# Optimization experiments

Measured on AMD Instinct MI355X. Metric: run time of the kernel, lower is better.

## Reference

```python
import jax, jax.numpy as jnp
import numpy as np

B = 512          # batch of visual features
VF_D = 4096      # visual feature dim (VGG fc7)
HID_D = 2048     # hidden dim
EMB_D = 300      # order-embedding / label-vector dim
N_LABELS = 2000  # number of GT label vectors


def setup_inputs() -> dict:
    key = jax.random.key(0)
    ks = jax.random.split(key, 4)
    vfs = jax.random.normal(ks[0], (B, VF_D), dtype=jnp.float32)
    W1 = jax.random.normal(ks[1], (VF_D, HID_D), dtype=jnp.float32) * (1.0 / np.sqrt(VF_D))
    b1 = jnp.zeros((HID_D,), dtype=jnp.float32)
    W2 = jax.random.normal(ks[2], (HID_D, EMB_D), dtype=jnp.float32) * (1.0 / np.sqrt(HID_D))
    b2 = jnp.zeros((EMB_D,), dtype=jnp.float32)
    gt_label_vecs = jax.random.normal(ks[3], (N_LABELS, EMB_D), dtype=jnp.float32)
    return {"vfs": vfs, "W1": W1, "b1": b1, "W2": W2, "b2": b2,
            "gt_label_vecs": gt_label_vecs}


def reference(vfs, W1, b1, W2, b2, gt_label_vecs):
    # hidden_layer: ReLU -> (Dropout, identity at eval) -> Linear
    vf_hidden = jnp.dot(jax.nn.relu(vfs), W1) + b1            # [B, HID_D]
    # embedding_layer: ReLU -> Linear
    vf_emb = jnp.dot(jax.nn.relu(vf_hidden), W2) + b2         # [B, EMB_D]
    # order_sim(hypers=gt_label_vecs, hypos=vf_emb):
    #   score = -|| clamp(hypo - hyper, min=0) ||^2, batched over all pairs
    diff = jax.nn.relu(vf_emb[:, None, :] - gt_label_vecs[None, :, :])  # [B, N, D]
    score_stack = -jnp.sum(diff * diff, axis=-1)              # [B, N_LABELS]
    return score_stack, vf_emb
```

## Files before the change

### kernel.cpp

```cpp
#include <hip/hip_runtime.h>

#define B_SZ   512
#define VFD    4096
#define HIDD   2048
#define EMBD   300
#define NLAB   2000
#define NPAD   320

#define G1_SPLIT 4
#define G2_SPLIT 8
#define SD_SPLIT 4

typedef __attribute__((ext_vector_type(8))) short short8x;
typedef __attribute__((ext_vector_type(4))) float f32x4;
typedef __attribute__((ext_vector_type(8))) unsigned short ushort8;
typedef __attribute__((ext_vector_type(4))) unsigned short ushort4x;

typedef const __attribute__((address_space(1))) unsigned int* gas_t;
typedef __attribute__((address_space(3))) unsigned int* las_t;

__device__ inline unsigned short f2bf(float x) {
    unsigned u = __float_as_uint(x);
    u += 0x7FFF + ((u >> 16) & 1);
    return (unsigned short)(u >> 16);
}

__global__ __launch_bounds__(256) void prep_kernel(
    const float* __restrict__ vfs, unsigned short* __restrict__ Xb,
    const float* __restrict__ W1, unsigned short* __restrict__ W1T,
    const float* __restrict__ W2, unsigned short* __restrict__ W2T)
{
    __shared__ float tile[64][65];
    const int tid = threadIdx.x;
    const int blk = blockIdx.x;

    if (blk < 1024) {
        const int i = (blk * 256 + tid) * 8;
        float4 a = *(const float4*)&vfs[i];
        float4 b = *(const float4*)&vfs[i + 4];
        ushort8 o;
        o[0] = f2bf(fmaxf(a.x, 0.f)); o[1] = f2bf(fmaxf(a.y, 0.f));
        o[2] = f2bf(fmaxf(a.z, 0.f)); o[3] = f2bf(fmaxf(a.w, 0.f));
        o[4] = f2bf(fmaxf(b.x, 0.f)); o[5] = f2bf(fmaxf(b.y, 0.f));
        o[6] = f2bf(fmaxf(b.z, 0.f)); o[7] = f2bf(fmaxf(b.w, 0.f));
        *(ushort8*)&Xb[i] = o;
        return;
    }

    const float* in; unsigned short* out; int N, ldK, bx, by;
    if (blk < 3072) {
        const int b = blk - 1024;
        in = W1; out = W1T; N = HIDD; ldK = VFD; bx = b & 31; by = b >> 5;
    } else {
        const int b = blk - 3072;
        in = W2; out = W2T; N = EMBD; ldK = HIDD; bx = b % 5; by = b / 5;
    }
    const int n0 = bx * 64, k0 = by * 64;

    #pragma unroll
    for (int i = 0; i < 4; ++i) {
        const int s = tid + 256 * i;
        const int kr = s >> 4, nc = (s & 15) * 4;
        float4 v = {0.f, 0.f, 0.f, 0.f};
        if (n0 + nc < N) v = *(const float4*)&in[(size_t)(k0 + kr) * N + n0 + nc];
        tile[kr][nc + 0] = v.x; tile[kr][nc + 1] = v.y;
        tile[kr][nc + 2] = v.z; tile[kr][nc + 3] = v.w;
    }
    __syncthreads();

    const int row = tid >> 2, kq = (tid & 3) * 16;
    ushort8 o0, o1;
    #pragma unroll
    for (int j = 0; j < 8; ++j) o0[j] = f2bf(tile[kq + j][row]);
    #pragma unroll
    for (int j = 0; j < 8; ++j) o1[j] = f2bf(tile[kq + 8 + j][row]);
    const size_t off = (size_t)(n0 + row) * ldK + k0 + kq;
    *(ushort8*)&out[off]     = o0;
    *(ushort8*)&out[off + 8] = o1;
}

__global__ __launch_bounds__(256) void gemm1_kernel(
    const unsigned short* __restrict__ A,
    const unsigned short* __restrict__ Bt,
    float* __restrict__ Cpart)
{
    __shared__ unsigned short As[2][2048];
    __shared__ unsigned short Bs[2][4096];

    const int tid = threadIdx.x;
    const int m0 = blockIdx.y * 64, n0 = blockIdx.x * 128;
    const int kbase = blockIdx.z * (VFD / G1_SPLIT);

    const unsigned short* ga = A + (size_t)(m0 + (tid & 63)) * VFD + kbase + (tid >> 6) * 8;
    const int brow = tid & 127, boct = tid >> 7;
    const unsigned short* gb0 = Bt + (size_t)(n0 + brow) * VFD + kbase + boct * 8;
    const unsigned short* gb1 = gb0 + 16;

    const int lane = tid & 63;
    const int wave = tid >> 6;
    const int wm = (wave & 1) * 32;
    const int wn = (wave >> 1) * 64;
    const int q = lane >> 4, l15 = lane & 15;

    f32x4 acc[2][4];
    #pragma unroll
    for (int r = 0; r < 2; ++r)
        #pragma unroll
        for (int c = 0; c < 4; ++c) acc[r][c] = (f32x4){0.f,0.f,0.f,0.f};

    __builtin_amdgcn_global_load_lds((gas_t)(const void*)ga,
                                     (las_t)(void*)&As[0][tid * 8], 16, 0, 0);
    __builtin_amdgcn_global_load_lds((gas_t)(const void*)gb0,
                                     (las_t)(void*)&Bs[0][tid * 8], 16, 0, 0);
    __builtin_amdgcn_global_load_lds((gas_t)(const void*)gb1,
                                     (las_t)(void*)&Bs[0][(tid + 256) * 8], 16, 0, 0);

    const int iters = (VFD / G1_SPLIT) / 32;
    for (int t = 0; t < iters; ++t) {
        const int cur = t & 1, nxt = cur ^ 1;
        __syncthreads();

        if (t + 1 < iters) {
            const int ko = (t + 1) * 32;
            __builtin_amdgcn_global_load_lds((gas_t)(const void*)(ga + ko),
                                             (las_t)(void*)&As[nxt][tid * 8], 16, 0, 0);
            __builtin_amdgcn_global_load_lds((gas_t)(const void*)(gb0 + ko),
                                             (las_t)(void*)&Bs[nxt][tid * 8], 16, 0, 0);
            __builtin_amdgcn_global_load_lds((gas_t)(const void*)(gb1 + ko),
                                             (las_t)(void*)&Bs[nxt][(tid + 256) * 8], 16, 0, 0);
        }

        short8x a0 = *(short8x*)&As[cur][(q * 64 + wm +      l15) * 8];
        short8x a1 = *(short8x*)&As[cur][(q * 64 + wm + 16 + l15) * 8];
        #pragma unroll
        for (int c = 0; c < 4; ++c) {
            short8x b = *(short8x*)&Bs[cur][(q * 128 + wn + c * 16 + l15) * 8];
            acc[0][c] = __builtin_amdgcn_mfma_f32_16x16x32_bf16(a0, b, acc[0][c], 0, 0, 0);
            acc[1][c] = __builtin_amdgcn_mfma_f32_16x16x32_bf16(a1, b, acc[1][c], 0, 0, 0);
        }
    }

    float* Cz = Cpart + (size_t)blockIdx.z * B_SZ * HIDD;
    #pragma unroll
    for (int r = 0; r < 2; ++r) {
        #pragma unroll
        for (int g = 0; g < 4; ++g) {
            const int rr = m0 + wm + r * 16 + q * 4 + g;
            #pragma unroll
            for (int c = 0; c < 4; ++c)
                Cz[(size_t)rr * HIDD + n0 + wn + c * 16 + l15] = acc[r][c][g];
        }
    }
}

template<int LDA, int LDB, int LDC, int KCHUNK>
__global__ __launch_bounds__(256) void gemm_bf16_kernel(
    const unsigned short* __restrict__ A,
    const unsigned short* __restrict__ Bt,
    float* __restrict__ Cpart, int M)
{
    __shared__ unsigned short As[2][2048];
    __shared__ unsigned short Bs[2][2048];

    const int tid = threadIdx.x;
    const int m0 = blockIdx.y * 64, n0 = blockIdx.x * 64;
    const int kbase = blockIdx.z * KCHUNK;

    const unsigned short* ga = A  + (size_t)(m0 + (tid & 63)) * LDA + kbase + (tid >> 6) * 8;
    const unsigned short* gb = Bt + (size_t)(n0 + (tid & 63)) * LDB + kbase + (tid >> 6) * 8;

    const int lane = tid & 63;
    const int wave = tid >> 6;
    const int wm = (wave & 1) * 32;
    const int wn = (wave >> 1) * 32;
    const int q = lane >> 4, l15 = lane & 15;

    f32x4 acc00 = {0.f,0.f,0.f,0.f}, acc01 = {0.f,0.f,0.f,0.f};
    f32x4 acc10 = {0.f,0.f,0.f,0.f}, acc11 = {0.f,0.f,0.f,0.f};

    __builtin_amdgcn_global_load_lds((gas_t)(const void*)ga,
                                     (las_t)(void*)&As[0][tid * 8], 16, 0, 0);
    __builtin_amdgcn_global_load_lds((gas_t)(const void*)gb,
                                     (las_t)(void*)&Bs[0][tid * 8], 16, 0, 0);

    const int iters = KCHUNK / 32;
    for (int t = 0; t < iters; ++t) {
        const int cur = t & 1, nxt = cur ^ 1;
        __syncthreads();

        if (t + 1 < iters) {
            __builtin_amdgcn_global_load_lds((gas_t)(const void*)(ga + (t + 1) * 32),
                                             (las_t)(void*)&As[nxt][tid * 8], 16, 0, 0);
            __builtin_amdgcn_global_load_lds((gas_t)(const void*)(gb + (t + 1) * 32),
                                             (las_t)(void*)&Bs[nxt][tid * 8], 16, 0, 0);
        }

        short8x a0 = *(short8x*)&As[cur][(q * 64 + wm +      l15) * 8];
        short8x a1 = *(short8x*)&As[cur][(q * 64 + wm + 16 + l15) * 8];
        short8x b0 = *(short8x*)&Bs[cur][(q * 64 + wn +      l15) * 8];
        short8x b1 = *(short8x*)&Bs[cur][(q * 64 + wn + 16 + l15) * 8];
        acc00 = __builtin_amdgcn_mfma_f32_16x16x32_bf16(a0, b0, acc00, 0, 0, 0);
        acc01 = __builtin_amdgcn_mfma_f32_16x16x32_bf16(a0, b1, acc01, 0, 0, 0);
        acc10 = __builtin_amdgcn_mfma_f32_16x16x32_bf16(a1, b0, acc10, 0, 0, 0);
        acc11 = __builtin_amdgcn_mfma_f32_16x16x32_bf16(a1, b1, acc11, 0, 0, 0);
    }

    float* Cz = Cpart + (size_t)blockIdx.z * M * LDC;
    #pragma unroll
    for (int r = 0; r < 4; ++r) {
        const int rr = m0 + wm + q * 4 + r;
        const int cc = n0 + wn + l15;
        Cz[(size_t)rr * LDC + cc]             = acc00[r];
        Cz[(size_t)rr * LDC + cc + 16]        = acc01[r];
        Cz[(size_t)(rr + 16) * LDC + cc]      = acc10[r];
        Cz[(size_t)(rr + 16) * LDC + cc + 16] = acc11[r];
    }
}

__global__ __launch_bounds__(256) void reduce_h_kernel(
    const float* __restrict__ Hpart, const float* __restrict__ b1,
    unsigned short* __restrict__ Hb)
{
    const int i = (blockIdx.x * 256 + threadIdx.x) * 4;
    const int col = i & (HIDD - 1);
    float4 s = *(const float4*)&b1[col];
    #pragma unroll
    for (int z = 0; z < G1_SPLIT; ++z) {
        float4 p = *(const float4*)&Hpart[(size_t)z * B_SZ * HIDD + i];
        s.x += p.x; s.y += p.y; s.z += p.z; s.w += p.w;
    }
    ushort4x o;
    o[0] = f2bf(fmaxf(s.x, 0.f));
    o[1] = f2bf(fmaxf(s.y, 0.f));
    o[2] = f2bf(fmaxf(s.z, 0.f));
    o[3] = f2bf(fmaxf(s.w, 0.f));
    *(ushort4x*)&Hb[i] = o;
}

__global__ __launch_bounds__(256) void reduce_e_zero_kernel(
    const float* __restrict__ Epart, const float* __restrict__ b2,
    float* __restrict__ E, float* __restrict__ scores)
{
    const int blk = blockIdx.x;
    if (blk < 600) {
        const int gid = blk * 256 + threadIdx.x;
        if (gid >= B_SZ * EMBD) return;
        const int m = gid / EMBD, n = gid - m * EMBD;
        float v = b2[n];
        #pragma unroll
        for (int z = 0; z < G2_SPLIT; ++z)
            v += Epart[(size_t)z * B_SZ * NPAD + m * NPAD + n];
        E[gid] = v;
    } else {
        const int i = ((blk - 600) * 256 + threadIdx.x) * 4;
        if (i < B_SZ * NLAB) {
            float4 z = {0.f, 0.f, 0.f, 0.f};
            *(float4*)&scores[i] = z;
        }
    }
}

__global__ __launch_bounds__(128) void scores_part_kernel(
    const float* __restrict__ E, const float* __restrict__ G,
    float* __restrict__ scores)
{
    __shared__ float Gs[64][44];

    const int tid = threadIdx.x;
    const int tx = tid & 15, ty = tid >> 4;
    const int n0 = blockIdx.x * 64, b0 = blockIdx.y * 32;
    const int dbase = blockIdx.z * (NPAD / SD_SPLIT);

    float acc[4][4] = {};

    for (int dc = 0; dc < NPAD / SD_SPLIT; dc += 40) {
        const int d0 = dbase + dc;
        __syncthreads();
        #pragma unroll
        for (int i = 0; i < 5; ++i) {
            const int s = tid + 128 * i;
            const int row = s / 10, qd = (s - row * 10) * 4;
            const int d = d0 + qd;
            const int n = n0 + row;
            float4 v = {0.f, 0.f, 0.f, 0.f};
            if (n < NLAB && d < EMBD) v = *(const float4*)&G[(size_t)n * EMBD + d];
            *(float4*)&Gs[row][qd] = v;
        }
        __syncthreads();

        #pragma unroll 2
        for (int d = 0; d < 40; d += 4) {
            const int dd = d0 + d;
            float4 e[4];
            if (dd < EMBD) {
                #pragma unroll
                for (int r = 0; r < 4; ++r)
                    e[r] = *(const float4*)&E[(size_t)(b0 + ty * 4 + r) * EMBD + dd];
            } else {
                #pragma unroll
                for (int r = 0; r < 4; ++r) e[r] = make_float4(0.f, 0.f, 0.f, 0.f);
            }
            #pragma unroll
            for (int c = 0; c < 4; ++c) {
                float4 g = *(float4*)&Gs[tx + 16 * c][d];
                #pragma unroll
                for (int r = 0; r < 4; ++r) {
                    float t;
                    t = fmaxf(e[r].x - g.x, 0.f); acc[r][c] += t * t;
                    t = fmaxf(e[r].y - g.y, 0.f); acc[r][c] += t * t;
                    t = fmaxf(e[r].z - g.z, 0.f); acc[r][c] += t * t;
                    t = fmaxf(e[r].w - g.w, 0.f); acc[r][c] += t * t;
                }
            }
        }
    }

    #pragma unroll
    for (int r = 0; r < 4; ++r) {
        const int b = b0 + ty * 4 + r;
        #pragma unroll
        for (int c = 0; c < 4; ++c) {
            const int n = n0 + tx + 16 * c;
            if (n < NLAB) atomicAdd(&scores[(size_t)b * NLAB + n], -acc[r][c]);
        }
    }
}

extern "C" void kernel_launch(void* const* d_in, const int* in_sizes, int n_in,
                              void* d_out, int out_size, void* d_ws, size_t ws_size,
                              hipStream_t stream)
{
    const float* vfs = (const float*)d_in[0];
    const float* W1  = (const float*)d_in[1];
    const float* b1  = (const float*)d_in[2];
    const float* W2  = (const float*)d_in[3];
    const float* b2  = (const float*)d_in[4];
    const float* G   = (const float*)d_in[5];

    float* out    = (float*)d_out;
    float* scores = out;
    float* E      = out + (size_t)B_SZ * NLAB;

    char* ws = (char*)d_ws;
    unsigned short* Xb  = (unsigned short*)(ws);
    unsigned short* W1T = (unsigned short*)(ws + 4194304);
    unsigned short* W2T = (unsigned short*)(ws + 20971520);
    unsigned short* Hb  = (unsigned short*)(ws + 22282240);
    float*          Hpart = (float*)(ws + 24379392);
    float*          Epart = (float*)(ws + 41156608);

    prep_kernel<<<3232, 256, 0, stream>>>(vfs, Xb, W1, W1T, W2, W2T);

    gemm1_kernel<<<dim3(16, 8, G1_SPLIT), 256, 0, stream>>>(Xb, W1T, Hpart);
    reduce_h_kernel<<<1024, 256, 0, stream>>>(Hpart, b1, Hb);

    gemm_bf16_kernel<HIDD, HIDD, NPAD, HIDD / G2_SPLIT>
        <<<dim3(5, 8, G2_SPLIT), 256, 0, stream>>>(Hb, W2T, Epart, B_SZ);
    reduce_e_zero_kernel<<<1624, 256, 0, stream>>>(Epart, b2, E, scores);

    scores_part_kernel<<<dim3(32, 16, SD_SPLIT), 128, 0, stream>>>(E, G, scores);
}
```

Measured before the change: 174.5 us.

## Deepen GEMM K-tiles to 64, pack bf16 in transpose, move score zeroing to prep

Both bf16 MFMA GEMMs now stage 64-wide K tiles per double-buffered iteration instead of 32. This halves the number of barriers and loop iterations at the cost of twice the LDS per block. The weight-transpose prep converts to bf16 before the LDS transpose, packing pairs of K values into 32-bit words, which cuts LDS footprint and shared-memory traffic. Zeroing of the score buffer moves from the E-reduction kernel into extra blocks of the prep kernel, so it runs off the critical path.

```diff
diff --git a/kernel.cpp b/kernel.cpp
--- a/kernel.cpp
+++ b/kernel.cpp
@@ -28,9 +28,10 @@
 __global__ __launch_bounds__(256) void prep_kernel(
     const float* __restrict__ vfs, unsigned short* __restrict__ Xb,
     const float* __restrict__ W1, unsigned short* __restrict__ W1T,
-    const float* __restrict__ W2, unsigned short* __restrict__ W2T)
-{
-    __shared__ float tile[64][65];
+    const float* __restrict__ W2, unsigned short* __restrict__ W2T,
+    float* __restrict__ scores)
+{
+    __shared__ unsigned int Lds[64][34];
     const int tid = threadIdx.x;
     const int blk = blockIdx.x;
 
@@ -46,6 +47,14 @@
         *(ushort8*)&Xb[i] = o;
         return;
     }
+    if (blk >= 3232) {
+        const int i = ((blk - 3232) * 256 + tid) * 4;
+        if (i < B_SZ * NLAB) {
+            float4 z = {0.f, 0.f, 0.f, 0.f};
+            *(float4*)&scores[i] = z;
+        }
+        return;
+    }
 
     const float* in; unsigned short* out; int N, ldK, bx, by;
     if (blk < 3072) {
@@ -58,25 +67,31 @@
     const int n0 = bx * 64, k0 = by * 64;
 
     #pragma unroll
-    for (int i = 0; i < 4; ++i) {
+    for (int i = 0; i < 2; ++i) {
         const int s = tid + 256 * i;
-        const int kr = s >> 4, nc = (s & 15) * 4;
-        float4 v = {0.f, 0.f, 0.f, 0.f};
-        if (n0 + nc < N) v = *(const float4*)&in[(size_t)(k0 + kr) * N + n0 + nc];
-        tile[kr][nc + 0] = v.x; tile[kr][nc + 1] = v.y;
-        tile[kr][nc + 2] = v.z; tile[kr][nc + 3] = v.w;
+        const int kp = s >> 4, nq = s & 15;
+        const int n = n0 + nq * 4;
+        float4 v0 = {0.f,0.f,0.f,0.f}, v1 = {0.f,0.f,0.f,0.f};
+        if (n < N) {
+            v0 = *(const float4*)&in[(size_t)(k0 + 2 * kp)     * N + n];
+            v1 = *(const float4*)&in[(size_t)(k0 + 2 * kp + 1) * N + n];
+        }
+        Lds[nq*4+0][kp] = (unsigned)f2bf(v0.x) | ((unsigned)f2bf(v1.x) << 16);
+        Lds[nq*4+1][kp] = (unsigned)f2bf(v0.y) | ((unsigned)f2bf(v1.y) << 16);
+        Lds[nq*4+2][kp] = (unsigned)f2bf(v0.z) | ((unsigned)f2bf(v1.z) << 16);
+        Lds[nq*4+3][kp] = (unsigned)f2bf(v0.w) | ((unsigned)f2bf(v1.w) << 16);
     }
     __syncthreads();
 
-    const int row = tid >> 2, kq = (tid & 3) * 16;
-    ushort8 o0, o1;
-    #pragma unroll
-    for (int j = 0; j < 8; ++j) o0[j] = f2bf(tile[kq + j][row]);
-    #pragma unroll
-    for (int j = 0; j < 8; ++j) o1[j] = f2bf(tile[kq + 8 + j][row]);
-    const size_t off = (size_t)(n0 + row) * ldK + k0 + kq;
-    *(ushort8*)&out[off]     = o0;
-    *(ushort8*)&out[off + 8] = o1;
+    #pragma unroll
+    for (int i = 0; i < 2; ++i) {
+        const int c = tid + 256 * i;
+        const int n = c >> 3, oct = c & 7;
+        uint2 lo = *(uint2*)&Lds[n][oct * 4];
+        uint2 hi = *(uint2*)&Lds[n][oct * 4 + 2];
+        uint4 v = make_uint4(lo.x, lo.y, hi.x, hi.y);
+        *(uint4*)&out[(size_t)(n0 + n) * ldK + k0 + oct * 8] = v;
+    }
 }
 
 __global__ __launch_bounds__(256) void gemm1_kernel(
@@ -84,17 +99,15 @@
     const unsigned short* __restrict__ Bt,
     float* __restrict__ Cpart)
 {
-    __shared__ unsigned short As[2][2048];
-    __shared__ unsigned short Bs[2][4096];
+    __shared__ unsigned short As[2][4096];
+    __shared__ unsigned short Bs[2][8192];
 
     const int tid = threadIdx.x;
     const int m0 = blockIdx.y * 64, n0 = blockIdx.x * 128;
     const int kbase = blockIdx.z * (VFD / G1_SPLIT);
 
     const unsigned short* ga = A + (size_t)(m0 + (tid & 63)) * VFD + kbase + (tid >> 6) * 8;
-    const int brow = tid & 127, boct = tid >> 7;
-    const unsigned short* gb0 = Bt + (size_t)(n0 + brow) * VFD + kbase + boct * 8;
-    const unsigned short* gb1 = gb0 + 16;
+    const unsigned short* gb = Bt + (size_t)(n0 + (tid & 127)) * VFD + kbase + (tid >> 7) * 8;
 
     const int lane = tid & 63;
     const int wave = tid >> 6;
@@ -108,35 +121,43 @@
         #pragma unroll
         for (int c = 0; c < 4; ++c) acc[r][c] = (f32x4){0.f,0.f,0.f,0.f};
 
-    __builtin_amdgcn_global_load_lds((gas_t)(const void*)ga,
-                                     (las_t)(void*)&As[0][tid * 8], 16, 0, 0);
-    __builtin_amdgcn_global_load_lds((gas_t)(const void*)gb0,
-                                     (las_t)(void*)&Bs[0][tid * 8], 16, 0, 0);
-    __builtin_amdgcn_global_load_lds((gas_t)(const void*)gb1,
-                                     (las_t)(void*)&Bs[0][(tid + 256) * 8], 16, 0, 0);
-
-    const int iters = (VFD / G1_SPLIT) / 32;
+    #pragma unroll
+    for (int i = 0; i < 2; ++i)
+        __builtin_amdgcn_global_load_lds((gas_t)(const void*)(ga + i * 32),
+                                         (las_t)(void*)&As[0][(tid + 256 * i) * 8], 16, 0, 0);
+    #pragma unroll
+    for (int i = 0; i < 4; ++i)
+        __builtin_amdgcn_global_load_lds((gas_t)(const void*)(gb + i * 16),
+                                         (las_t)(void*)&Bs[0][(tid + 256 * i) * 8], 16, 0, 0);
+
+    const int iters = (VFD / G1_SPLIT) / 64;
     for (int t = 0; t < iters; ++t) {
         const int cur = t & 1, nxt = cur ^ 1;
         __syncthreads();
 
         if (t + 1 < iters) {
-            const int ko = (t + 1) * 32;
-            __builtin_amdgcn_global_load_lds((gas_t)(const void*)(ga + ko),
-                                             (las_t)(void*)&As[nxt][tid * 8], 16, 0, 0);
-            __builtin_amdgcn_global_load_lds((gas_t)(const void*)(gb0 + ko),
-                                             (las_t)(void*)&Bs[nxt][tid * 8], 16, 0, 0);
-            __builtin_amdgcn_global_load_lds((gas_t)(const void*)(gb1 + ko),
-                                             (las_t)(void*)&Bs[nxt][(tid + 256) * 8], 16, 0, 0);
-        }
-
-        short8x a0 = *(short8x*)&As[cur][(q * 64 + wm +      l15) * 8];
-        short8x a1 = *(short8x*)&As[cur][(q * 64 + wm + 16 + l15) * 8];
-        #pragma unroll
-        for (int c = 0; c < 4; ++c) {
-            short8x b = *(short8x*)&Bs[cur][(q * 128 + wn + c * 16 + l15) * 8];
-            acc[0][c] = __builtin_amdgcn_mfma_f32_16x16x32_bf16(a0, b, acc[0][c], 0, 0, 0);
-            acc[1][c] = __builtin_amdgcn_mfma_f32_16x16x32_bf16(a1, b, acc[1][c], 0, 0, 0);
+            const int ko = (t + 1) * 64;
+            #pragma unroll
+            for (int i = 0; i < 2; ++i)
+                __builtin_amdgcn_global_load_lds((gas_t)(const void*)(ga + ko + i * 32),
+                                                 (las_t)(void*)&As[nxt][(tid + 256 * i) * 8], 16, 0, 0);
+            #pragma unroll
+            for (int i = 0; i < 4; ++i)
+                __builtin_amdgcn_global_load_lds((gas_t)(const void*)(gb + ko + i * 16),
+                                                 (las_t)(void*)&Bs[nxt][(tid + 256 * i) * 8], 16, 0, 0);
+        }
+
+        #pragma unroll
+        for (int kk = 0; kk < 2; ++kk) {
+            const int oct = kk * 4 + q;
+            short8x a0 = *(short8x*)&As[cur][(oct * 64 + wm +      l15) * 8];
+            short8x a1 = *(short8x*)&As[cur][(oct * 64 + wm + 16 + l15) * 8];
+            #pragma unroll
+            for (int c = 0; c < 4; ++c) {
+                short8x b = *(short8x*)&Bs[cur][(oct * 128 + wn + c * 16 + l15) * 8];
+                acc[0][c] = __builtin_amdgcn_mfma_f32_16x16x32_bf16(a0, b, acc[0][c], 0, 0, 0);
+                acc[1][c] = __builtin_amdgcn_mfma_f32_16x16x32_bf16(a1, b, acc[1][c], 0, 0, 0);
+            }
         }
     }
 
@@ -159,8 +180,8 @@
     const unsigned short* __restrict__ Bt,
     float* __restrict__ Cpart, int M)
 {
-    __shared__ unsigned short As[2][2048];
-    __shared__ unsigned short Bs[2][2048];
+    __shared__ unsigned short As[2][4096];
+    __shared__ unsigned short Bs[2][4096];
 
     const int tid = threadIdx.x;
     const int m0 = blockIdx.y * 64, n0 = blockIdx.x * 64;
@@ -178,31 +199,42 @@
     f32x4 acc00 = {0.f,0.f,0.f,0.f}, acc01 = {0.f,0.f,0.f,0.f};
     f32x4 acc10 = {0.f,0.f,0.f,0.f}, acc11 = {0.f,0.f,0.f,0.f};
 
-    __builtin_amdgcn_global_load_lds((gas_t)(const void*)ga,
-                                     (las_t)(void*)&As[0][tid * 8], 16, 0, 0);
-    __builtin_amdgcn_global_load_lds((gas_t)(const void*)gb,
-                                     (las_t)(void*)&Bs[0][tid * 8], 16, 0, 0);
-
-    const int iters = KCHUNK / 32;
+    #pragma unroll
+    for (int i = 0; i < 2; ++i) {
+        __builtin_amdgcn_global_load_lds((gas_t)(const void*)(ga + i * 32),
+                                         (las_t)(void*)&As[0][(tid + 256 * i) * 8], 16, 0, 0);
+        __builtin_amdgcn_global_load_lds((gas_t)(const void*)(gb + i * 32),
+                                         (las_t)(void*)&Bs[0][(tid + 256 * i) * 8], 16, 0, 0);
+    }
+
+    const int iters = KCHUNK / 64;
     for (int t = 0; t < iters; ++t) {
         const int cur = t & 1, nxt = cur ^ 1;
         __syncthreads();
 
         if (t + 1 < iters) {
-            __builtin_amdgcn_global_load_lds((gas_t)(const void*)(ga + (t + 1) * 32),
-                                             (las_t)(void*)&As[nxt][tid * 8], 16, 0, 0);
-            __builtin_amdgcn_global_load_lds((gas_t)(const void*)(gb + (t + 1) * 32),
-                                             (las_t)(void*)&Bs[nxt][tid * 8], 16, 0, 0);
-        }
-
-        short8x a0 = *(short8x*)&As[cur][(q * 64 + wm +      l15) * 8];
-        short8x a1 = *(short8x*)&As[cur][(q * 64 + wm + 16 + l15) * 8];
-        short8x b0 = *(short8x*)&Bs[cur][(q * 64 + wn +      l15) * 8];
-        short8x b1 = *(short8x*)&Bs[cur][(q * 64 + wn + 16 + l15) * 8];
-        acc00 = __builtin_amdgcn_mfma_f32_16x16x32_bf16(a0, b0, acc00, 0, 0, 0);
-        acc01 = __builtin_amdgcn_mfma_f32_16x16x32_bf16(a0, b1, acc01, 0, 0, 0);
-        acc10 = __builtin_amdgcn_mfma_f32_16x16x32_bf16(a1, b0, acc10, 0, 0, 0);
-        acc11 = __builtin_amdgcn_mfma_f32_16x16x32_bf16(a1, b1, acc11, 0, 0, 0);
+            const int ko = (t + 1) * 64;
+            #pragma unroll
+            for (int i = 0; i < 2; ++i) {
+                __builtin_amdgcn_global_load_lds((gas_t)(const void*)(ga + ko + i * 32),
+                                                 (las_t)(void*)&As[nxt][(tid + 256 * i) * 8], 16, 0, 0);
+                __builtin_amdgcn_global_load_lds((gas_t)(const void*)(gb + ko + i * 32),
+                                                 (las_t)(void*)&Bs[nxt][(tid + 256 * i) * 8], 16, 0, 0);
+            }
+        }
+
+        #pragma unroll
+        for (int kk = 0; kk < 2; ++kk) {
+            const int oct = kk * 4 + q;
+            short8x a0 = *(short8x*)&As[cur][(oct * 64 + wm +      l15) * 8];
+            short8x a1 = *(short8x*)&As[cur][(oct * 64 + wm + 16 + l15) * 8];
+            short8x b0 = *(short8x*)&Bs[cur][(oct * 64 + wn +      l15) * 8];
+            short8x b1 = *(short8x*)&Bs[cur][(oct * 64 + wn + 16 + l15) * 8];
+            acc00 = __builtin_amdgcn_mfma_f32_16x16x32_bf16(a0, b0, acc00, 0, 0, 0);
+            acc01 = __builtin_amdgcn_mfma_f32_16x16x32_bf16(a0, b1, acc01, 0, 0, 0);
+            acc10 = __builtin_amdgcn_mfma_f32_16x16x32_bf16(a1, b0, acc10, 0, 0, 0);
+            acc11 = __builtin_amdgcn_mfma_f32_16x16x32_bf16(a1, b1, acc11, 0, 0, 0);
+        }
     }
 
     float* Cz = Cpart + (size_t)blockIdx.z * M * LDC;
@@ -237,27 +269,18 @@
     *(ushort4x*)&Hb[i] = o;
 }
 
-__global__ __launch_bounds__(256) void reduce_e_zero_kernel(
+__global__ __launch_bounds__(256) void reduce_e_kernel(
     const float* __restrict__ Epart, const float* __restrict__ b2,
-    float* __restrict__ E, float* __restrict__ scores)
-{
-    const int blk = blockIdx.x;
-    if (blk < 600) {
-        const int gid = blk * 256 + threadIdx.x;
-        if (gid >= B_SZ * EMBD) return;
-        const int m = gid / EMBD, n = gid - m * EMBD;
-        float v = b2[n];
-        #pragma unroll
-        for (int z = 0; z < G2_SPLIT; ++z)
-            v += Epart[(size_t)z * B_SZ * NPAD + m * NPAD + n];
-        E[gid] = v;
-    } else {
-        const int i = ((blk - 600) * 256 + threadIdx.x) * 4;
-        if (i < B_SZ * NLAB) {
-            float4 z = {0.f, 0.f, 0.f, 0.f};
-            *(float4*)&scores[i] = z;
-        }
-    }
+    float* __restrict__ E)
+{
+    const int gid = blockIdx.x * 256 + threadIdx.x;
+    if (gid >= B_SZ * EMBD) return;
+    const int m = gid / EMBD, n = gid - m * EMBD;
+    float v = b2[n];
+    #pragma unroll
+    for (int z = 0; z < G2_SPLIT; ++z)
+        v += Epart[(size_t)z * B_SZ * NPAD + m * NPAD + n];
+    E[gid] = v;
 }
 
 __global__ __launch_bounds__(128) void scores_part_kernel(
@@ -349,14 +372,14 @@
     float*          Hpart = (float*)(ws + 24379392);
     float*          Epart = (float*)(ws + 41156608);
 
-    prep_kernel<<<3232, 256, 0, stream>>>(vfs, Xb, W1, W1T, W2, W2T);
+    prep_kernel<<<4256, 256, 0, stream>>>(vfs, Xb, W1, W1T, W2, W2T, scores);
 
     gemm1_kernel<<<dim3(16, 8, G1_SPLIT), 256, 0, stream>>>(Xb, W1T, Hpart);
     reduce_h_kernel<<<1024, 256, 0, stream>>>(Hpart, b1, Hb);
 
     gemm_bf16_kernel<HIDD, HIDD, NPAD, HIDD / G2_SPLIT>
         <<<dim3(5, 8, G2_SPLIT), 256, 0, stream>>>(Hb, W2T, Epart, B_SZ);
-    reduce_e_zero_kernel<<<1624, 256, 0, stream>>>(Epart, b2, E, scores);
+    reduce_e_kernel<<<600, 256, 0, stream>>>(Epart, b2, E);
 
     scores_part_kernel<<<dim3(32, 16, SD_SPLIT), 128, 0, stream>>>(E, G, scores);
 }
```

Measured after the change: 170.2 us. 2.5% less time.
